# Optimization experiments

Measured on AMD Instinct MI355X. Metric: run time of the kernel, lower is better.

## Reference

```python
import jax, jax.numpy as jnp
import numpy as np

GRID_SIZE = 8
SCALE_SPLINE = 0.1
BATCH, IN_F, OUT_F = 2048, 1024, 1024


def setup_inputs() -> dict:
    key = jax.random.key(0)
    k1, k2, k3 = jax.random.split(key, 3)
    x = jax.random.normal(k1, (BATCH, IN_F), dtype=jnp.float32)
    # kaiming-uniform-ish scale for base linear weight
    bound = 1.0 / np.sqrt(IN_F)
    base_weight = jax.random.uniform(k2, (OUT_F, IN_F), dtype=jnp.float32,
                                     minval=-bound, maxval=bound)
    spline_coeff = 0.1 * jax.random.normal(k3, (OUT_F, IN_F, GRID_SIZE), dtype=jnp.float32)
    # grid buffer: identical linspace(-1,1,G+1) for every (out,in); keep 1-D
    grid = jnp.linspace(-1.0, 1.0, GRID_SIZE + 1, dtype=jnp.float32)
    return {"x": x, "base_weight": base_weight, "spline_coeff": spline_coeff, "grid": grid}


def reference(x, base_weight, spline_coeff, grid):
    # x: (B, I); base_weight: (O, I); spline_coeff: (O, I, G); grid: (G+1,)
    G = spline_coeff.shape[-1]
    base_out = x @ base_weight.T                       # (B, O)

    xc = jnp.clip(x, -1.0, 1.0)                        # (B, I)
    # bucketize: number of grid knots <= xc, minus 1, clamped to valid bin
    mask = xc[..., None] >= grid                       # (B, I, G+1)
    left_idx = jnp.clip(mask.sum(axis=-1) - 1, 0, G - 1)  # (B, I) int

    left_grid = grid[left_idx]                         # (B, I)
    right_grid = grid[left_idx + 1]                    # (B, I)
    denom = right_grid - left_grid
    denom = jnp.where(denom == 0, jnp.ones_like(denom), denom)
    weight = (xc - left_grid) / denom                  # (B, I)

    # coeff gather + weighted sum over in_features, expressed as a dense
    # contraction against a weight-scaled one-hot of the bin index:
    # spline_out[b,o] = sum_i spline_coeff[o,i,idx[b,i]] * weight[b,i]
    onehot_w = jax.nn.one_hot(left_idx, G, dtype=x.dtype) * weight[..., None]  # (B, I, G)
    spline_out = jnp.einsum('big,oig->bo', onehot_w, spline_coeff)             # (B, O)

    return base_out + SCALE_SPLINE * spline_out
```

## Files before the change

### kernel.cpp

```cpp
#include <hip/hip_runtime.h>
#include <stdint.h>

#define BATCH 2048
#define INF 1024
#define OUTF 1024
#define GRID_G 8
#define KTOT 9216

#define SK 8
#define MTT 8
#define NTT 4
#define CSLAB ((size_t)BATCH * OUTF)

typedef __attribute__((ext_vector_type(8))) short short8_t;
typedef __attribute__((ext_vector_type(4))) float f32x4_t;
typedef __attribute__((ext_vector_type(8))) unsigned short u16x8_t;

__device__ __forceinline__ unsigned short f2bf(float f) {
  unsigned int u = __float_as_uint(f);
  u += 0x7FFFu + ((u >> 16) & 1u);
  return (unsigned short)(u >> 16);
}

__device__ __forceinline__ void async16(void* lds, const void* g) {
  __builtin_amdgcn_global_load_lds(
      (const __attribute__((address_space(1))) void*)g,
      (__attribute__((address_space(3))) void*)lds, 16, 0, 0);
}

__device__ __forceinline__ short8_t onehot_frag(unsigned int p) {
  unsigned int wlo = p & 0xFFFFu;
  unsigned int idx = p >> 16;
  unsigned int sel = (idx & 1u) ? (wlo << 16) : wlo;
  unsigned int jt = idx >> 1;
  union { unsigned int u[4]; short8_t s; } r;
  r.u[0] = (jt == 0u) ? sel : 0u;
  r.u[1] = (jt == 1u) ? sel : 0u;
  r.u[2] = (jt == 2u) ? sel : 0u;
  r.u[3] = (jt == 3u) ? sel : 0u;
  return r.s;
}

__global__ __launch_bounds__(256) void build_w_kernel(
    const float* __restrict__ bw, const float* __restrict__ coeff,
    unsigned short* __restrict__ wc) {
  int id = blockIdx.x * 256 + threadIdx.x;
  int row = id / (KTOT / 8);
  int k8 = id - row * (KTOT / 8);
  int k = k8 * 8;
  const float* src = (k < INF) ? (bw + (size_t)row * INF + k)
                               : (coeff + (size_t)row * (INF * GRID_G) + (k - INF));
  const float4* s4 = (const float4*)src;
  float4 a = s4[0], b = s4[1];
  u16x8_t v;
  v[0] = f2bf(a.x); v[1] = f2bf(a.y); v[2] = f2bf(a.z); v[3] = f2bf(a.w);
  v[4] = f2bf(b.x); v[5] = f2bf(b.y); v[6] = f2bf(b.z); v[7] = f2bf(b.w);
  *(u16x8_t*)(wc + (size_t)id * 8) = v;
}

__global__ __launch_bounds__(256) void build_apack_kernel(
    const float* __restrict__ x, const float* __restrict__ grid,
    unsigned short* __restrict__ xbf, unsigned int* __restrict__ ap) {
  __shared__ float sg[GRID_G + 1];
  if (threadIdx.x <= GRID_G) sg[threadIdx.x] = grid[threadIdx.x];
  __syncthreads();
  int id = blockIdx.x * 256 + threadIdx.x;
  float xv = x[id];
  xbf[id] = f2bf(xv);
  float xc = fminf(fmaxf(xv, -1.0f), 1.0f);
  int cnt = 0;
#pragma unroll
  for (int j = 0; j <= GRID_G; ++j) cnt += (xc >= sg[j]) ? 1 : 0;
  int idx = cnt - 1;
  idx = idx < 0 ? 0 : (idx > GRID_G - 1 ? GRID_G - 1 : idx);
  float left = sg[idx], right = sg[idx + 1];
  float denom = right - left;
  denom = (denom == 0.0f) ? 1.0f : denom;
  float w = (xc - left) / denom;
  ap[id] = (unsigned int)f2bf(0.1f * w) | ((unsigned int)idx << 16);
}

__global__ __launch_bounds__(512, 2) void fused_gemm_kernel(
    const unsigned short* __restrict__ Xb, const unsigned int* __restrict__ Ap,
    const unsigned short* __restrict__ Wc, unsigned short* __restrict__ P) {
  __shared__ unsigned short LA[2][2][256 * 32];
  __shared__ unsigned short LB[2][2][256 * 32];

  int bid = blockIdx.x;
  int sk = bid & 7;
  int t0i = bid >> 3;
  int mt = t0i >> 2, nt = t0i & 3;

  int tid = threadIdx.x, wave = tid >> 6, lane = tid & 63;
  int wr = wave >> 2, wc = wave & 3;
  int lr = lane & 15, lk = lane >> 4;
  int rlo = lk * 128 + lr * 8;

  int srow = wave * 16 + (lane & 15);
  int scol = ((lane >> 4) & 3) * 8;
  const unsigned short* gXA  = Xb + (size_t)(mt * 256 + srow) * INF + sk * 128 + scol;
  const unsigned short* gXA2 = gXA + (size_t)128 * INF;
  const unsigned short* gB   = Wc + (size_t)(nt * 256 + srow) * KTOT + scol;
  const unsigned short* gB2  = gB + (size_t)128 * KTOT;
  const unsigned int* gAP = Ap + (size_t)(mt * 256 + wave * 32 + (lane >> 1)) * INF
                            + sk * 128 + (lane & 1) * 4;

  unsigned int* APK0 = (unsigned int*)&LA[0][0][0];
  unsigned int* APK1 = (unsigned int*)&LA[1][0][0];

  const int CB = sk * 128;
  const int CS = 1024 + sk * 1024;

  f32x4_t acc[2][4][4];
#pragma unroll
  for (int ch = 0; ch < 2; ++ch)
#pragma unroll
    for (int mf = 0; mf < 4; ++mf)
#pragma unroll
      for (int nf = 0; nf < 4; ++nf) acc[ch][mf][nf] = f32x4_t{0.f, 0.f, 0.f, 0.f};

#define VMW(N) asm volatile("s_waitcnt vmcnt(" #N ")" ::: "memory")
#define BARR() { __builtin_amdgcn_s_barrier(); asm volatile("" ::: "memory"); }
#define STAGE_XA(nb, ks, colofs) { unsigned short* d_ = &LA[nb][ks][wave * 512]; \
    async16(d_, gXA + (colofs) + (ks) * 32); \
    async16(d_ + 4096, gXA2 + (colofs) + (ks) * 32); }
#define STAGE_B(nb, ks, colofs) { unsigned short* d_ = &LB[nb][ks][wave * 512]; \
    async16(d_, gB + (colofs) + (ks) * 32); \
    async16(d_ + 4096, gB2 + (colofs) + (ks) * 32); }
#define STAGE_APK(APKn, tt) { async16((void*)((APKn) + wave * 256), gAP + ((tt) - 2) * 8); }
#define DSR_A(af_, CC, ks, ch) { _Pragma("unroll") for (int mf = 0; mf < 4; ++mf) \
    af_[mf] = *(const short8_t*)&LA[CC][ks][(wr * 8 + (ch) * 4 + mf) * 512 + rlo]; }
#define DSR_B(bf_, CC, ks) { _Pragma("unroll") for (int nf = 0; nf < 4; ++nf) \
    bf_[nf] = *(const short8_t*)&LB[CC][ks][(wc * 4 + nf) * 512 + rlo]; }
#define PRD(pr_, APKc, ks, ch) { _Pragma("unroll") for (int mf = 0; mf < 4; ++mf) \
    pr_[mf] = (APKc)[(wr * 128 + (ch) * 64 + mf * 16 + lr) * 8 + (ks) * 4 + lk]; }
#define EXPAND(af_, pr_) { _Pragma("unroll") for (int mf = 0; mf < 4; ++mf) \
    af_[mf] = onehot_frag(pr_[mf]); }
#define MFMA16(CH, af_, bf_) { __builtin_amdgcn_s_setprio(1); \
    _Pragma("unroll") for (int mf = 0; mf < 4; ++mf) \
    _Pragma("unroll") for (int nf = 0; nf < 4; ++nf) \
      acc[CH][mf][nf] = __builtin_amdgcn_mfma_f32_16x16x32_bf16( \
          af_[mf], bf_[nf], acc[CH][mf][nf], 0, 0, 0); \
    __builtin_amdgcn_s_setprio(0); }

  STAGE_XA(0, 0, 0) STAGE_B(0, 0, CB) STAGE_XA(0, 1, 0) STAGE_B(0, 1, CB)

  {
    short8_t af[4], bf[4];
    VMW(4); BARR();
    DSR_A(af, 0, 0, 0) DSR_B(bf, 0, 0)
    STAGE_XA(1, 0, 64)
    MFMA16(0, af, bf)
    DSR_A(af, 0, 0, 1)
    STAGE_B(1, 0, CB + 64)
    MFMA16(1, af, bf)
    VMW(4); BARR();
    DSR_A(af, 0, 1, 0) DSR_B(bf, 0, 1)
    STAGE_XA(1, 1, 64)
    MFMA16(0, af, bf)
    DSR_A(af, 0, 1, 1)
    STAGE_B(1, 1, CB + 64)
    MFMA16(1, af, bf)
  }
  {
    short8_t af[4], bf[4];
    VMW(4); BARR();
    DSR_A(af, 1, 0, 0) DSR_B(bf, 1, 0)
    STAGE_APK(APK0, 2)
    MFMA16(0, af, bf)
    DSR_A(af, 1, 0, 1)
    STAGE_B(0, 0, CS)
    MFMA16(1, af, bf)
    VMW(3); BARR();
    DSR_A(af, 1, 1, 0) DSR_B(bf, 1, 1)
    STAGE_B(0, 1, CS)
    MFMA16(0, af, bf)
    DSR_A(af, 1, 1, 1)
    MFMA16(1, af, bf)
  }
  for (int t = 2; t < 18; ++t) {
    int c = t & 1;
    unsigned int* APKc = c ? APK1 : APK0;
    unsigned int* APKn = c ? APK0 : APK1;
    int nb = c ^ 1;
    bool pf = t < 17;
    int cs = CS + (t - 1) * 64;
    short8_t af[4], bf[4];
    unsigned int pr[4];
    VMW(2); BARR();
    PRD(pr, APKc, 0, 0) DSR_B(bf, c, 0)
    if (pf) STAGE_APK(APKn, t + 1)
    EXPAND(af, pr) MFMA16(0, af, bf)
    PRD(pr, APKc, 0, 1)
    if (pf) STAGE_B(nb, 0, cs)
    EXPAND(af, pr) MFMA16(1, af, bf)
    if (pf) { VMW(3); } else { VMW(0); }
    BARR();
    PRD(pr, APKc, 1, 0) DSR_B(bf, c, 1)
    if (pf) STAGE_B(nb, 1, cs)
    EXPAND(af, pr) MFMA16(0, af, bf)
    PRD(pr, APKc, 1, 1)
    EXPAND(af, pr) MFMA16(1, af, bf)
  }

  unsigned short* slab = P + (size_t)sk * CSLAB;
#pragma unroll
  for (int ch = 0; ch < 2; ++ch)
#pragma unroll
    for (int mf = 0; mf < 4; ++mf)
#pragma unroll
      for (int nf = 0; nf < 4; ++nf) {
        int col = nt * 256 + wc * 64 + nf * 16 + lr;
        int rowb = mt * 256 + wr * 128 + ch * 64 + mf * 16 + lk * 4;
#pragma unroll
        for (int r = 0; r < 4; ++r)
          slab[(size_t)(rowb + r) * OUTF + col] = f2bf(acc[ch][mf][nf][r]);
      }
}

__global__ __launch_bounds__(256) void reduce_kernel(
    const unsigned short* __restrict__ P, float* __restrict__ out) {
  size_t base = ((size_t)blockIdx.x * 256 + threadIdx.x) * 8;
  float s[8];
#pragma unroll
  for (int j = 0; j < 8; ++j) s[j] = 0.0f;
#pragma unroll
  for (int k = 0; k < SK; ++k) {
    u16x8_t v = *(const u16x8_t*)(P + (size_t)k * CSLAB + base);
#pragma unroll
    for (int j = 0; j < 8; ++j)
      s[j] += __uint_as_float((unsigned int)v[j] << 16);
  }
  float4 lo = {s[0], s[1], s[2], s[3]};
  float4 hi = {s[4], s[5], s[6], s[7]};
  *(float4*)(out + base) = lo;
  *(float4*)(out + base + 4) = hi;
}

extern "C" void kernel_launch(void* const* d_in, const int* in_sizes, int n_in,
                              void* d_out, int out_size, void* d_ws, size_t ws_size,
                              hipStream_t stream) {
  const float* x = (const float*)d_in[0];
  const float* bw = (const float*)d_in[1];
  const float* coeff = (const float*)d_in[2];
  const float* grid = (const float*)d_in[3];
  float* out = (float*)d_out;

  unsigned short* Wcat = (unsigned short*)d_ws;
  unsigned short* Xbf  = Wcat + (size_t)OUTF * KTOT;
  unsigned int*   Apack = (unsigned int*)(Xbf + (size_t)BATCH * INF);
  unsigned short* Part = (unsigned short*)(Apack + (size_t)BATCH * INF);

  build_w_kernel<<<OUTF * (KTOT / 8) / 256, 256, 0, stream>>>(bw, coeff, Wcat);
  build_apack_kernel<<<BATCH * INF / 256, 256, 0, stream>>>(x, grid, Xbf, Apack);
  fused_gemm_kernel<<<SK * MTT * NTT, 512, 0, stream>>>(Xbf, Apack, Wcat, Part);
  reduce_kernel<<<(int)(CSLAB / 8 / 256), 256, 0, stream>>>(Part, out);
}
```

Measured before the change: 71.33 us.

## Fuse split-K reduction into GEMM via last-block atomic counter

Removes the separate reduce kernel. Each GEMM block now bumps a per-tile atomic counter after writing its partial slab, and the last of the SK blocks for a tile sums all partial slabs and writes the fp32 output. The block index mapping also changes so split-K slices of the same tile are spread apart in launch order. This saves a kernel launch and lets the reduction overlap with GEMM tail work. In exchange it adds a memset, thread fences, and a serialized reduction tail inside the last block of each tile.

```diff
diff --git a/kernel.cpp b/kernel.cpp
--- a/kernel.cpp
+++ b/kernel.cpp
@@ -20,6 +20,10 @@
   unsigned int u = __float_as_uint(f);
   u += 0x7FFFu + ((u >> 16) & 1u);
   return (unsigned short)(u >> 16);
+}
+
+__device__ __forceinline__ float bf2f(unsigned short h) {
+  return __uint_as_float((unsigned int)h << 16);
 }
 
 __device__ __forceinline__ void async16(void* lds, const void* g) {
@@ -82,13 +86,14 @@
 
 __global__ __launch_bounds__(512, 2) void fused_gemm_kernel(
     const unsigned short* __restrict__ Xb, const unsigned int* __restrict__ Ap,
-    const unsigned short* __restrict__ Wc, unsigned short* __restrict__ P) {
+    const unsigned short* __restrict__ Wc, unsigned short* __restrict__ P,
+    int* __restrict__ tc, float* __restrict__ out) {
   __shared__ unsigned short LA[2][2][256 * 32];
   __shared__ unsigned short LB[2][2][256 * 32];
 
   int bid = blockIdx.x;
-  int sk = bid & 7;
-  int t0i = bid >> 3;
+  int sk = bid >> 5;
+  int t0i = bid & 31;
   int mt = t0i >> 2, nt = t0i & 3;
 
   int tid = threadIdx.x, wave = tid >> 6, lane = tid & 63;
@@ -216,25 +221,33 @@
         for (int r = 0; r < 4; ++r)
           slab[(size_t)(rowb + r) * OUTF + col] = f2bf(acc[ch][mf][nf][r]);
       }
-}
-
-__global__ __launch_bounds__(256) void reduce_kernel(
-    const unsigned short* __restrict__ P, float* __restrict__ out) {
-  size_t base = ((size_t)blockIdx.x * 256 + threadIdx.x) * 8;
-  float s[8];
-#pragma unroll
-  for (int j = 0; j < 8; ++j) s[j] = 0.0f;
-#pragma unroll
-  for (int k = 0; k < SK; ++k) {
-    u16x8_t v = *(const u16x8_t*)(P + (size_t)k * CSLAB + base);
-#pragma unroll
-    for (int j = 0; j < 8; ++j)
-      s[j] += __uint_as_float((unsigned int)v[j] << 16);
-  }
-  float4 lo = {s[0], s[1], s[2], s[3]};
-  float4 hi = {s[4], s[5], s[6], s[7]};
-  *(float4*)(out + base) = lo;
-  *(float4*)(out + base + 4) = hi;
+
+  __threadfence();
+  __shared__ int lastflag;
+  if (tid == 0) lastflag = (atomicAdd(&tc[t0i], 1) == SK - 1) ? 1 : 0;
+  __syncthreads();
+  if (lastflag) {
+    __threadfence();
+#pragma unroll 1
+    for (int cch = 0; cch < 16; ++cch) {
+      int rl = cch * 16 + (tid >> 5);
+      int cl = (tid & 31) * 8;
+      size_t base = (size_t)(mt * 256 + rl) * OUTF + nt * 256 + cl;
+      float s8[8];
+#pragma unroll
+      for (int j = 0; j < 8; ++j) s8[j] = 0.0f;
+#pragma unroll
+      for (int s = 0; s < SK; ++s) {
+        u16x8_t v = *(const u16x8_t*)(P + (size_t)s * CSLAB + base);
+#pragma unroll
+        for (int j = 0; j < 8; ++j) s8[j] += bf2f(v[j]);
+      }
+      float4 lo = {s8[0], s8[1], s8[2], s8[3]};
+      float4 hi = {s8[4], s8[5], s8[6], s8[7]};
+      *(float4*)(out + base) = lo;
+      *(float4*)(out + base + 4) = hi;
+    }
+  }
 }
 
 extern "C" void kernel_launch(void* const* d_in, const int* in_sizes, int n_in,
@@ -250,9 +263,10 @@
   unsigned short* Xbf  = Wcat + (size_t)OUTF * KTOT;
   unsigned int*   Apack = (unsigned int*)(Xbf + (size_t)BATCH * INF);
   unsigned short* Part = (unsigned short*)(Apack + (size_t)BATCH * INF);
-
+  int* tcnt = (int*)(Part + (size_t)SK * CSLAB);
+
+  hipMemsetAsync(tcnt, 0, 32 * sizeof(int), stream);
   build_w_kernel<<<OUTF * (KTOT / 8) / 256, 256, 0, stream>>>(bw, coeff, Wcat);
   build_apack_kernel<<<BATCH * INF / 256, 256, 0, stream>>>(x, grid, Xbf, Apack);
-  fused_gemm_kernel<<<SK * MTT * NTT, 512, 0, stream>>>(Xbf, Apack, Wcat, Part);
-  reduce_kernel<<<(int)(CSLAB / 8 / 256), 256, 0, stream>>>(Part, out);
-}
+  fused_gemm_kernel<<<SK * MTT * NTT, 512, 0, stream>>>(Xbf, Apack, Wcat, Part, tcnt, out);
+}
```

Measured after the change: 165.3 us. 132% more time.
